# Optimization experiments

Hardware: AMD Instinct MI355X
Metric: run time of the kernel (lower is better)

Reference implementation:

```python
import jax, jax.numpy as jnp
import numpy as np

S, B, H = 4096, 32, 512

def setup_inputs() -> dict:
    key = jax.random.key(0)
    k1, k2, k3, k4, k5 = jax.random.split(key, 5)
    hidden = jax.random.normal(k1, (1, B, H), dtype=jnp.float32)
    encoder_outputs = jax.random.normal(k2, (S, B, H), dtype=jnp.float32)
    embedding = jax.random.normal(k3, (S, B, 3), dtype=jnp.float32)
    # learned params (xavier-ish scale)
    bigram_matrix = jax.random.normal(k4, (H, H), dtype=jnp.float32) * (1.0 / np.sqrt(H))
    affect_matrix = jax.random.normal(k5, (H, 3), dtype=jnp.float32) * 0.1
    return {"hidden": hidden, "encoder_outputs": encoder_outputs,
            "embedding": embedding, "bigram_matrix": bigram_matrix,
            "affect_matrix": affect_matrix}

def reference(hidden, encoder_outputs, embedding, bigram_matrix, affect_matrix):
    # hidden: [1,B,H] -> [B,H] (view(-1) over single layer)
    h = hidden[0]
    # bigram-modulated encoder states:
    #   i == 0: enc[0]
    #   i  > 0: (enc[i-1] @ W_bigram) * enc[i]
    modulated = jnp.einsum('sbh,hk->sbk', encoder_outputs[:-1], bigram_matrix) * encoder_outputs[1:]
    bigram_hidden = jnp.concatenate([encoder_outputs[:1], modulated], axis=0)  # [S,B,H]
    # dot-attention energy per (b, s)
    e_dot = jnp.einsum('sbh,bh->bs', bigram_hidden, h)  # [B,S]
    # affect term: (h @ affect_matrix) . embedding[s,b]
    e_aff = jnp.einsum('bk,sbk->bs', jnp.einsum('bh,hk->bk', h, affect_matrix), embedding)
    attn = jax.nn.softmax(e_dot + e_aff, axis=-1)  # softmax over seq dim
    return attn[:, None, :]  # [B,1,S]
```

## Files before the change

### kernel.cpp

```cpp
#include <hip/hip_runtime.h>
#include <cstdint>
#include <cstddef>

#define S_DIM 4096
#define B_DIM 32
#define H_DIM 512
#define M_DIM (S_DIM * B_DIM)

typedef unsigned short u16;
typedef unsigned int u32;
typedef float f32x4 __attribute__((ext_vector_type(4)));
typedef __bf16 bf16x8 __attribute__((ext_vector_type(8)));

__device__ __forceinline__ u16 f2bf(float v) {
    union { float f; u32 u; } a; a.f = v;
    u32 r = a.u + 0x7fffu + ((a.u >> 16) & 1u);
    return (u16)(r >> 16);
}
__device__ __forceinline__ float bf2f(u16 b) {
    union { float f; u32 u; } a; a.u = ((u32)b) << 16; return a.f;
}
__device__ __forceinline__ void split_bf(float v, u16& h, u16& l) {
    h = f2bf(v);
    l = f2bf(v - bf2f(h));
}

__device__ __forceinline__ void gl2lds16(const void* g, void* l) {
    __builtin_amdgcn_global_load_lds(
        (const __attribute__((address_space(1))) unsigned int*)g,
        (__attribute__((address_space(3))) unsigned int*)l,
        16, 0, 0);
}

__global__ void prep_w(const float* __restrict__ W,
                       u16* __restrict__ Wh, u16* __restrict__ Wl) {
    int i = blockIdx.x * 256 + threadIdx.x;
    float w = W[i];
    u16 h, l;
    split_bf(w, h, l);
    Wh[i] = h; Wl[i] = l;
}

__global__ void prep_v(const float* __restrict__ enc,
                       const float* __restrict__ hid,
                       u16* __restrict__ vh, u16* __restrict__ vl,
                       int m_base, int m_count) {
    const size_t nq = (size_t)m_count * (H_DIM / 4);
    const size_t stride = (size_t)gridDim.x * 256;
    for (size_t i = blockIdx.x * 256 + threadIdx.x; i < nq; i += stride) {
        const size_t elem  = i * 4;
        const size_t gelem = (size_t)m_base * H_DIM + elem;
        const int k = (int)(gelem & (H_DIM - 1));
        const int b = (int)((gelem >> 9) & 31);
        const float4 e = *(const float4*)(enc + gelem);
        const float4 h = *(const float4*)(hid + b * H_DIM + k);
        float v0 = e.x * h.x, v1 = e.y * h.y, v2 = e.z * h.z, v3 = e.w * h.w;
        u16 h0,h1,h2,h3,l0,l1,l2,l3;
        split_bf(v0, h0, l0); split_bf(v1, h1, l1);
        split_bf(v2, h2, l2); split_bf(v3, h3, l3);
        ushort4 hw, lw;
        hw.x = h0; hw.y = h1; hw.z = h2; hw.w = h3;
        lw.x = l0; lw.y = l1; lw.z = l2; lw.w = l3;
        *(ushort4*)(vh + elem) = hw;
        *(ushort4*)(vl + elem) = lw;
    }
}

__global__ __launch_bounds__(256, 2) void bigram_gemm(
    const float* __restrict__ enc,
    const u16* __restrict__ vh, const u16* __restrict__ vl,
    const u16* __restrict__ Wh, const u16* __restrict__ Wl,
    float* __restrict__ Lp, int m_base)
{
    __shared__ u16 sAh[128 * 32];
    __shared__ u16 sAl[128 * 32];
    __shared__ u16 sBh[128 * 32];
    __shared__ u16 sBl[128 * 32];
    __shared__ float rowsum[2][128];

    const int tid  = threadIdx.x;
    const int wave = tid >> 6;
    const int lane = tid & 63;
    const int wr   = wave >> 1;
    const int wc   = wave & 1;
    const int jt   = blockIdx.x & 3;
    const int mt   = blockIdx.x >> 2;
    const int m0   = m_base + mt * 128;
    const int j0   = jt * 128;
    const int g    = lane >> 4;
    const int cl   = lane & 15;

    const int srow = wave * 32 + (lane >> 2);
    const int scol = (lane & 3) * 8;
    const size_t aoff0 = (size_t)(mt * 128 + srow) * H_DIM + scol;
    const size_t aoff1 = aoff0 + (size_t)16 * H_DIM;
    const size_t boff0 = (size_t)(j0 + srow) * H_DIM + scol;
    const size_t boff1 = boff0 + (size_t)16 * H_DIM;
    const u16* pAh0 = vh + aoff0; const u16* pAh1 = vh + aoff1;
    const u16* pAl0 = vl + aoff0; const u16* pAl1 = vl + aoff1;
    const u16* pBh0 = Wh + boff0; const u16* pBh1 = Wh + boff1;
    const u16* pBl0 = Wl + boff0; const u16* pBl1 = Wl + boff1;
    const int d0 = wave * 1024, d1 = wave * 1024 + 512;

    f32x4 acc[4][4];
    #pragma unroll
    for (int mf = 0; mf < 4; ++mf)
        #pragma unroll
        for (int nf = 0; nf < 4; ++nf)
            acc[mf][nf] = (f32x4){0.f, 0.f, 0.f, 0.f};

    for (int kt = 0; kt < 16; ++kt) {
        const int ko = kt * 32;
        __syncthreads();
        gl2lds16(pAh0 + ko, sAh + d0);
        gl2lds16(pAh1 + ko, sAh + d1);
        gl2lds16(pAl0 + ko, sAl + d0);
        gl2lds16(pAl1 + ko, sAl + d1);
        gl2lds16(pBh0 + ko, sBh + d0);
        gl2lds16(pBh1 + ko, sBh + d1);
        gl2lds16(pBl0 + ko, sBl + d0);
        gl2lds16(pBl1 + ko, sBl + d1);
        __syncthreads();

        bf16x8 ah[4], al[4], bh[4], bl[4];
        #pragma unroll
        for (int mf = 0; mf < 4; ++mf) {
            const int ar = wr * 64 + mf * 16 + cl;
            ah[mf] = *(const bf16x8*)(sAh + ar * 32 + g * 8);
            al[mf] = *(const bf16x8*)(sAl + ar * 32 + g * 8);
        }
        #pragma unroll
        for (int nf = 0; nf < 4; ++nf) {
            const int br = wc * 64 + nf * 16 + cl;
            bh[nf] = *(const bf16x8*)(sBh + br * 32 + g * 8);
            bl[nf] = *(const bf16x8*)(sBl + br * 32 + g * 8);
        }
        #pragma unroll
        for (int mf = 0; mf < 4; ++mf)
            #pragma unroll
            for (int nf = 0; nf < 4; ++nf) {
                acc[mf][nf] = __builtin_amdgcn_mfma_f32_16x16x32_bf16(ah[mf], bh[nf], acc[mf][nf], 0, 0, 0);
                acc[mf][nf] = __builtin_amdgcn_mfma_f32_16x16x32_bf16(ah[mf], bl[nf], acc[mf][nf], 0, 0, 0);
                acc[mf][nf] = __builtin_amdgcn_mfma_f32_16x16x32_bf16(al[mf], bh[nf], acc[mf][nf], 0, 0, 0);
            }
    }

    #pragma unroll
    for (int mf = 0; mf < 4; ++mf) {
        float rs0 = 0.f, rs1 = 0.f, rs2 = 0.f, rs3 = 0.f;
        const int growb = m0 + wr * 64 + mf * 16 + g * 4;
        #pragma unroll
        for (int nf = 0; nf < 4; ++nf) {
            const int gcol = j0 + wc * 64 + nf * 16 + cl;
            float e0 = (growb + 0 >= B_DIM) ? enc[(size_t)(growb + 0 - B_DIM) * H_DIM + gcol] : 0.f;
            float e1 = (growb + 1 >= B_DIM) ? enc[(size_t)(growb + 1 - B_DIM) * H_DIM + gcol] : 0.f;
            float e2 = (growb + 2 >= B_DIM) ? enc[(size_t)(growb + 2 - B_DIM) * H_DIM + gcol] : 0.f;
            float e3 = (growb + 3 >= B_DIM) ? enc[(size_t)(growb + 3 - B_DIM) * H_DIM + gcol] : 0.f;
            rs0 += acc[mf][nf][0] * e0;
            rs1 += acc[mf][nf][1] * e1;
            rs2 += acc[mf][nf][2] * e2;
            rs3 += acc[mf][nf][3] * e3;
        }
        #pragma unroll
        for (int off = 1; off < 16; off <<= 1) {
            rs0 += __shfl_xor(rs0, off);
            rs1 += __shfl_xor(rs1, off);
            rs2 += __shfl_xor(rs2, off);
            rs3 += __shfl_xor(rs3, off);
        }
        if (cl == 0) {
            const int rb = wr * 64 + mf * 16 + g * 4;
            rowsum[wc][rb + 0] = rs0;
            rowsum[wc][rb + 1] = rs1;
            rowsum[wc][rb + 2] = rs2;
            rowsum[wc][rb + 3] = rs3;
        }
    }
    __syncthreads();
    if (tid < 128) {
        const int gm = m0 + tid;
        if (gm >= B_DIM) {
            Lp[(size_t)jt * M_DIM + (size_t)(gm & 31) * S_DIM + (gm >> 5)] =
                rowsum[0][tid] + rowsum[1][tid];
        }
    }
}

__global__ __launch_bounds__(256, 2) void bigram_gemm_direct(
    const float* __restrict__ enc,
    const float* __restrict__ hid,
    const u16* __restrict__ Wh,
    const u16* __restrict__ Wl,
    float* __restrict__ Lp)
{
    __shared__ float rowsum[2][128];
    const int tid  = threadIdx.x;
    const int wave = tid >> 6;
    const int lane = tid & 63;
    const int wr   = wave >> 1;
    const int wc   = wave & 1;
    const int jt   = blockIdx.x & 3;
    const int m0   = (blockIdx.x >> 2) * 128;
    const int j0   = jt * 128;
    const int g    = lane >> 4;
    const int cl   = lane & 15;

    f32x4 acc[4][4];
    #pragma unroll
    for (int mf = 0; mf < 4; ++mf)
        #pragma unroll
        for (int nf = 0; nf < 4; ++nf)
            acc[mf][nf] = (f32x4){0.f, 0.f, 0.f, 0.f};

    for (int kt = 0; kt < 8; ++kt) {
        #pragma unroll
        for (int kk = 0; kk < 2; ++kk) {
            const int k0 = kt * 64 + kk * 32 + g * 8;
            const float4 hA0 = *(const float4*)(hid + (size_t)cl * H_DIM + k0);
            const float4 hA1 = *(const float4*)(hid + (size_t)cl * H_DIM + k0 + 4);
            const float4 hB0 = *(const float4*)(hid + (size_t)(cl + 16) * H_DIM + k0);
            const float4 hB1 = *(const float4*)(hid + (size_t)(cl + 16) * H_DIM + k0 + 4);
            bf16x8 ah[4], al[4];
            #pragma unroll
            for (int mf = 0; mf < 4; ++mf) {
                const size_t rbase = (size_t)(m0 + wr * 64 + mf * 16 + cl) * H_DIM + k0;
                const float4 e0 = *(const float4*)(enc + rbase);
                const float4 e1 = *(const float4*)(enc + rbase + 4);
                const float4 h0 = (mf & 1) ? hB0 : hA0;
                const float4 h1 = (mf & 1) ? hB1 : hA1;
                float v[8];
                v[0] = e0.x * h0.x; v[1] = e0.y * h0.y; v[2] = e0.z * h0.z; v[3] = e0.w * h0.w;
                v[4] = e1.x * h1.x; v[5] = e1.y * h1.y; v[6] = e1.z * h1.z; v[7] = e1.w * h1.w;
                union { bf16x8 v8; u16 s[8]; } Hi, Lo;
                #pragma unroll
                for (int i = 0; i < 8; ++i) split_bf(v[i], Hi.s[i], Lo.s[i]);
                ah[mf] = Hi.v8;
                al[mf] = Lo.v8;
            }
            bf16x8 bh[4], bl[4];
            #pragma unroll
            for (int nf = 0; nf < 4; ++nf) {
                const size_t roff = (size_t)(j0 + wc * 64 + nf * 16 + cl) * H_DIM + k0;
                bh[nf] = *(const bf16x8*)(Wh + roff);
                bl[nf] = *(const bf16x8*)(Wl + roff);
            }
            #pragma unroll
            for (int mf = 0; mf < 4; ++mf)
                #pragma unroll
                for (int nf = 0; nf < 4; ++nf) {
                    acc[mf][nf] = __builtin_amdgcn_mfma_f32_16x16x32_bf16(ah[mf], bh[nf], acc[mf][nf], 0, 0, 0);
                    acc[mf][nf] = __builtin_amdgcn_mfma_f32_16x16x32_bf16(ah[mf], bl[nf], acc[mf][nf], 0, 0, 0);
                    acc[mf][nf] = __builtin_amdgcn_mfma_f32_16x16x32_bf16(al[mf], bh[nf], acc[mf][nf], 0, 0, 0);
                }
        }
    }

    #pragma unroll
    for (int mf = 0; mf < 4; ++mf) {
        float rs0 = 0.f, rs1 = 0.f, rs2 = 0.f, rs3 = 0.f;
        const int growb = m0 + wr * 64 + mf * 16 + g * 4;
        #pragma unroll
        for (int nf = 0; nf < 4; ++nf) {
            const int gcol = j0 + wc * 64 + nf * 16 + cl;
            float e0 = (growb + 0 >= B_DIM) ? enc[(size_t)(growb + 0 - B_DIM) * H_DIM + gcol] : 0.f;
            float e1 = (growb + 1 >= B_DIM) ? enc[(size_t)(growb + 1 - B_DIM) * H_DIM + gcol] : 0.f;
            float e2 = (growb + 2 >= B_DIM) ? enc[(size_t)(growb + 2 - B_DIM) * H_DIM + gcol] : 0.f;
            float e3 = (growb + 3 >= B_DIM) ? enc[(size_t)(growb + 3 - B_DIM) * H_DIM + gcol] : 0.f;
            rs0 += acc[mf][nf][0] * e0;
            rs1 += acc[mf][nf][1] * e1;
            rs2 += acc[mf][nf][2] * e2;
            rs3 += acc[mf][nf][3] * e3;
        }
        #pragma unroll
        for (int off = 1; off < 16; off <<= 1) {
            rs0 += __shfl_xor(rs0, off);
            rs1 += __shfl_xor(rs1, off);
            rs2 += __shfl_xor(rs2, off);
            rs3 += __shfl_xor(rs3, off);
        }
        if (cl == 0) {
            const int rb = wr * 64 + mf * 16 + g * 4;
            rowsum[wc][rb + 0] = rs0;
            rowsum[wc][rb + 1] = rs1;
            rowsum[wc][rb + 2] = rs2;
            rowsum[wc][rb + 3] = rs3;
        }
    }
    __syncthreads();
    if (tid < 128) {
        const int gm = m0 + tid;
        if (gm >= B_DIM) {
            Lp[(size_t)jt * M_DIM + (size_t)(gm & 31) * S_DIM + (gm >> 5)] =
                rowsum[0][tid] + rowsum[1][tid];
        }
    }
}

__global__ __launch_bounds__(1024) void softmax_kernel(
    const float* __restrict__ enc,
    const float* __restrict__ hid,
    const float* __restrict__ emb,
    const float* __restrict__ aff,
    const float* __restrict__ Lp,
    float* __restrict__ out)
{
    __shared__ float logits[S_DIM];
    __shared__ float wred[16][4];
    __shared__ float bcast[4];
    __shared__ float wtmp[16];

    const int b    = blockIdx.x;
    const int tid  = threadIdx.x;
    const int wave = tid >> 6;
    const int lane = tid & 63;

    float p0 = 0.f, p1 = 0.f, p2 = 0.f, p3 = 0.f;
    if (tid < H_DIM) {
        const int h = tid;
        const float hv = hid[b * H_DIM + h];
        p0 = hv * aff[h * 3 + 0];
        p1 = hv * aff[h * 3 + 1];
        p2 = hv * aff[h * 3 + 2];
        p3 = hv * enc[(size_t)b * H_DIM + h];
    }
    #pragma unroll
    for (int off = 32; off > 0; off >>= 1) {
        p0 += __shfl_down(p0, off);
        p1 += __shfl_down(p1, off);
        p2 += __shfl_down(p2, off);
        p3 += __shfl_down(p3, off);
    }
    if (lane == 0) { wred[wave][0] = p0; wred[wave][1] = p1; wred[wave][2] = p2; wred[wave][3] = p3; }
    __syncthreads();
    if (tid < 4) {
        float s = 0.f;
        #pragma unroll
        for (int w = 0; w < 16; ++w) s += wred[w][tid];
        bcast[tid] = s;
    }
    __syncthreads();
    const float ha0 = bcast[0], ha1 = bcast[1], ha2 = bcast[2], s0dot = bcast[3];

    float mx = -3.4e38f;
    #pragma unroll
    for (int it = 0; it < 4; ++it) {
        const int s = tid + it * 1024;
        const size_t base = (size_t)b * S_DIM + s;
        const float ed = (s == 0) ? s0dot
            : (Lp[base] + Lp[(size_t)M_DIM + base] + Lp[2 * (size_t)M_DIM + base] + Lp[3 * (size_t)M_DIM + base]);
        const float* e = emb + (size_t)(s * B_DIM + b) * 3;
        const float lg = ed + ha0 * e[0] + ha1 * e[1] + ha2 * e[2];
        logits[s] = lg;
        mx = fmaxf(mx, lg);
    }
    #pragma unroll
    for (int off = 32; off > 0; off >>= 1) mx = fmaxf(mx, __shfl_xor(mx, off));
    if (lane == 0) wtmp[wave] = mx;
    __syncthreads();
    mx = wtmp[0];
    #pragma unroll
    for (int w = 1; w < 16; ++w) mx = fmaxf(mx, wtmp[w]);
    __syncthreads();

    float sum = 0.f;
    #pragma unroll
    for (int it = 0; it < 4; ++it) {
        const int s = tid + it * 1024;
        const float ex = __expf(logits[s] - mx);
        logits[s] = ex;
        sum += ex;
    }
    #pragma unroll
    for (int off = 32; off > 0; off >>= 1) sum += __shfl_xor(sum, off);
    if (lane == 0) wtmp[wave] = sum;
    __syncthreads();
    sum = 0.f;
    #pragma unroll
    for (int w = 0; w < 16; ++w) sum += wtmp[w];
    const float inv = 1.0f / sum;
    #pragma unroll
    for (int it = 0; it < 4; ++it) {
        const int s = tid + it * 1024;
        out[(size_t)b * S_DIM + s] = logits[s] * inv;
    }
}

extern "C" void kernel_launch(void* const* d_in, const int* in_sizes, int n_in,
                              void* d_out, int out_size, void* d_ws, size_t ws_size,
                              hipStream_t stream) {
    const float* hid = (const float*)d_in[0];
    const float* enc = (const float*)d_in[1];
    const float* emb = (const float*)d_in[2];
    const float* Wm  = (const float*)d_in[3];
    const float* aff = (const float*)d_in[4];
    float* out = (float*)d_out;

    char* ws = (char*)d_ws;
    u16*   Wh = (u16*)ws;
    u16*   Wl = (u16*)(ws + (512u << 10));
    float* Lp = (float*)(ws + (1024u << 10));
    char*  vbase = ws + (1024u << 10) + (size_t)4 * M_DIM * 4;
    const size_t fixed = (1024u << 10) + (size_t)4 * M_DIM * 4;

    hipLaunchKernelGGL(prep_w, dim3(1024), dim3(256), 0, stream, Wm, Wh, Wl);

    const size_t avail = (ws_size > fixed) ? ws_size - fixed : 0;
    long chunk_m = (long)((avail / 2048) / 128) * 128;
    if (chunk_m > M_DIM) chunk_m = M_DIM;

    if (chunk_m >= 128) {
        u16* vh = (u16*)vbase;
        u16* vl = (u16*)(vbase + (size_t)chunk_m * H_DIM * sizeof(u16));
        for (long m_base = 0; m_base < M_DIM; m_base += chunk_m) {
            long mc = M_DIM - m_base;
            if (mc > chunk_m) mc = chunk_m;
            hipLaunchKernelGGL(prep_v, dim3((u32)(mc / 16)), dim3(256), 0, stream,
                               enc, hid, vh, vl, (int)m_base, (int)mc);
            hipLaunchKernelGGL(bigram_gemm, dim3((u32)((mc / 128) * 4)), dim3(256), 0, stream,
                               enc, vh, vl, Wh, Wl, Lp, (int)m_base);
        }
    } else {
        hipLaunchKernelGGL(bigram_gemm_direct, dim3(4096), dim3(256), 0, stream,
                           enc, hid, Wh, Wl, Lp);
    }

    hipLaunchKernelGGL(softmax_kernel, dim3(32), dim3(1024), 0, stream,
                       enc, hid, emb, aff, Lp, out);
}
```

Baseline: 646.0 us.

## Widen bigram GEMM tile to 128x256 using 32x32x16 MFMA

The bigram GEMM now gives each block a 128x256 output tile instead of 128x128, so only two column tiles cover H. The inner product uses 32x32x16 bf16 MFMA instructions in place of 16x16x32, and the epilogue reduction is adapted to the 32x32 accumulator layout. This halves redundant reloads of the A operand and the number of partial sums the softmax kernel must add, which now takes the partial count as a parameter. In exchange the kernel uses more LDS and registers per block, which can lower occupancy.

```diff
diff --git a/kernel.cpp b/kernel.cpp
--- a/kernel.cpp
+++ b/kernel.cpp
@@ -10,6 +10,7 @@
 typedef unsigned short u16;
 typedef unsigned int u32;
 typedef float f32x4 __attribute__((ext_vector_type(4)));
+typedef float f32x16 __attribute__((ext_vector_type(16)));
 typedef __bf16 bf16x8 __attribute__((ext_vector_type(8)));
 
 __device__ __forceinline__ u16 f2bf(float v) {
@@ -74,8 +75,8 @@
 {
     __shared__ u16 sAh[128 * 32];
     __shared__ u16 sAl[128 * 32];
-    __shared__ u16 sBh[128 * 32];
-    __shared__ u16 sBl[128 * 32];
+    __shared__ u16 sBh[256 * 32];
+    __shared__ u16 sBl[256 * 32];
     __shared__ float rowsum[2][128];
 
     const int tid  = threadIdx.x;
@@ -83,97 +84,96 @@
     const int lane = tid & 63;
     const int wr   = wave >> 1;
     const int wc   = wave & 1;
-    const int jt   = blockIdx.x & 3;
-    const int mt   = blockIdx.x >> 2;
+    const int jt   = blockIdx.x & 1;
+    const int mt   = blockIdx.x >> 1;
     const int m0   = m_base + mt * 128;
-    const int j0   = jt * 128;
-    const int g    = lane >> 4;
-    const int cl   = lane & 15;
-
-    const int srow = wave * 32 + (lane >> 2);
+    const int j0   = jt * 256;
+    const int l31  = lane & 31;
+    const int lh   = lane >> 5;
+
+    const int srow = lane >> 2;
     const int scol = (lane & 3) * 8;
-    const size_t aoff0 = (size_t)(mt * 128 + srow) * H_DIM + scol;
+    const size_t aoff0 = (size_t)(mt * 128 + wave * 32 + srow) * H_DIM + scol;
     const size_t aoff1 = aoff0 + (size_t)16 * H_DIM;
-    const size_t boff0 = (size_t)(j0 + srow) * H_DIM + scol;
-    const size_t boff1 = boff0 + (size_t)16 * H_DIM;
-    const u16* pAh0 = vh + aoff0; const u16* pAh1 = vh + aoff1;
-    const u16* pAl0 = vl + aoff0; const u16* pAl1 = vl + aoff1;
-    const u16* pBh0 = Wh + boff0; const u16* pBh1 = Wh + boff1;
-    const u16* pBl0 = Wl + boff0; const u16* pBl1 = Wl + boff1;
-    const int d0 = wave * 1024, d1 = wave * 1024 + 512;
-
-    f32x4 acc[4][4];
-    #pragma unroll
-    for (int mf = 0; mf < 4; ++mf)
-        #pragma unroll
-        for (int nf = 0; nf < 4; ++nf)
-            acc[mf][nf] = (f32x4){0.f, 0.f, 0.f, 0.f};
+    const size_t boff  = (size_t)(j0 + wave * 64 + srow) * H_DIM + scol;
+    const int da = wave * 1024;
+    const int db = wave * 2048;
+
+    f32x16 acc[2][4];
+    #pragma unroll
+    for (int rb = 0; rb < 2; ++rb)
+        #pragma unroll
+        for (int cb = 0; cb < 4; ++cb)
+            #pragma unroll
+            for (int r = 0; r < 16; ++r)
+                acc[rb][cb][r] = 0.f;
 
     for (int kt = 0; kt < 16; ++kt) {
         const int ko = kt * 32;
         __syncthreads();
-        gl2lds16(pAh0 + ko, sAh + d0);
-        gl2lds16(pAh1 + ko, sAh + d1);
-        gl2lds16(pAl0 + ko, sAl + d0);
-        gl2lds16(pAl1 + ko, sAl + d1);
-        gl2lds16(pBh0 + ko, sBh + d0);
-        gl2lds16(pBh1 + ko, sBh + d1);
-        gl2lds16(pBl0 + ko, sBl + d0);
-        gl2lds16(pBl1 + ko, sBl + d1);
+        gl2lds16(vh + aoff0 + ko, sAh + da);
+        gl2lds16(vh + aoff1 + ko, sAh + da + 512);
+        gl2lds16(vl + aoff0 + ko, sAl + da);
+        gl2lds16(vl + aoff1 + ko, sAl + da + 512);
+        #pragma unroll
+        for (int q = 0; q < 4; ++q) {
+            gl2lds16(Wh + boff + (size_t)(q * 16) * H_DIM + ko, sBh + db + q * 512);
+            gl2lds16(Wl + boff + (size_t)(q * 16) * H_DIM + ko, sBl + db + q * 512);
+        }
         __syncthreads();
 
-        bf16x8 ah[4], al[4], bh[4], bl[4];
-        #pragma unroll
-        for (int mf = 0; mf < 4; ++mf) {
-            const int ar = wr * 64 + mf * 16 + cl;
-            ah[mf] = *(const bf16x8*)(sAh + ar * 32 + g * 8);
-            al[mf] = *(const bf16x8*)(sAl + ar * 32 + g * 8);
-        }
-        #pragma unroll
-        for (int nf = 0; nf < 4; ++nf) {
-            const int br = wc * 64 + nf * 16 + cl;
-            bh[nf] = *(const bf16x8*)(sBh + br * 32 + g * 8);
-            bl[nf] = *(const bf16x8*)(sBl + br * 32 + g * 8);
-        }
-        #pragma unroll
-        for (int mf = 0; mf < 4; ++mf)
-            #pragma unroll
-            for (int nf = 0; nf < 4; ++nf) {
-                acc[mf][nf] = __builtin_amdgcn_mfma_f32_16x16x32_bf16(ah[mf], bh[nf], acc[mf][nf], 0, 0, 0);
-                acc[mf][nf] = __builtin_amdgcn_mfma_f32_16x16x32_bf16(ah[mf], bl[nf], acc[mf][nf], 0, 0, 0);
-                acc[mf][nf] = __builtin_amdgcn_mfma_f32_16x16x32_bf16(al[mf], bh[nf], acc[mf][nf], 0, 0, 0);
-            }
-    }
-
-    #pragma unroll
-    for (int mf = 0; mf < 4; ++mf) {
-        float rs0 = 0.f, rs1 = 0.f, rs2 = 0.f, rs3 = 0.f;
-        const int growb = m0 + wr * 64 + mf * 16 + g * 4;
-        #pragma unroll
-        for (int nf = 0; nf < 4; ++nf) {
-            const int gcol = j0 + wc * 64 + nf * 16 + cl;
-            float e0 = (growb + 0 >= B_DIM) ? enc[(size_t)(growb + 0 - B_DIM) * H_DIM + gcol] : 0.f;
-            float e1 = (growb + 1 >= B_DIM) ? enc[(size_t)(growb + 1 - B_DIM) * H_DIM + gcol] : 0.f;
-            float e2 = (growb + 2 >= B_DIM) ? enc[(size_t)(growb + 2 - B_DIM) * H_DIM + gcol] : 0.f;
-            float e3 = (growb + 3 >= B_DIM) ? enc[(size_t)(growb + 3 - B_DIM) * H_DIM + gcol] : 0.f;
-            rs0 += acc[mf][nf][0] * e0;
-            rs1 += acc[mf][nf][1] * e1;
-            rs2 += acc[mf][nf][2] * e2;
-            rs3 += acc[mf][nf][3] * e3;
-        }
-        #pragma unroll
-        for (int off = 1; off < 16; off <<= 1) {
-            rs0 += __shfl_xor(rs0, off);
-            rs1 += __shfl_xor(rs1, off);
-            rs2 += __shfl_xor(rs2, off);
-            rs3 += __shfl_xor(rs3, off);
-        }
-        if (cl == 0) {
-            const int rb = wr * 64 + mf * 16 + g * 4;
-            rowsum[wc][rb + 0] = rs0;
-            rowsum[wc][rb + 1] = rs1;
-            rowsum[wc][rb + 2] = rs2;
-            rowsum[wc][rb + 3] = rs3;
+        #pragma unroll
+        for (int ks = 0; ks < 2; ++ks) {
+            const int kb = ks * 16 + lh * 8;
+            bf16x8 ah[2], al[2], bh[4], bl[4];
+            #pragma unroll
+            for (int rb = 0; rb < 2; ++rb) {
+                const int row = wr * 64 + rb * 32 + l31;
+                ah[rb] = *(const bf16x8*)(sAh + row * 32 + kb);
+                al[rb] = *(const bf16x8*)(sAl + row * 32 + kb);
+            }
+            #pragma unroll
+            for (int cb = 0; cb < 4; ++cb) {
+                const int row = wc * 128 + cb * 32 + l31;
+                bh[cb] = *(const bf16x8*)(sBh + row * 32 + kb);
+                bl[cb] = *(const bf16x8*)(sBl + row * 32 + kb);
+            }
+            #pragma unroll
+            for (int rb = 0; rb < 2; ++rb)
+                #pragma unroll
+                for (int cb = 0; cb < 4; ++cb) {
+                    acc[rb][cb] = __builtin_amdgcn_mfma_f32_32x32x16_bf16(ah[rb], bh[cb], acc[rb][cb], 0, 0, 0);
+                    acc[rb][cb] = __builtin_amdgcn_mfma_f32_32x32x16_bf16(ah[rb], bl[cb], acc[rb][cb], 0, 0, 0);
+                    acc[rb][cb] = __builtin_amdgcn_mfma_f32_32x32x16_bf16(al[rb], bh[cb], acc[rb][cb], 0, 0, 0);
+                }
+        }
+    }
+
+    #pragma unroll
+    for (int rb = 0; rb < 2; ++rb) {
+        float t[16];
+        #pragma unroll
+        for (int r = 0; r < 16; ++r) {
+            const int rloc = (r & 3) + 8 * (r >> 2) + 4 * lh;
+            const int grow = m0 + wr * 64 + rb * 32 + rloc;
+            float tv = 0.f;
+            if (grow >= B_DIM) {
+                const float* ep = enc + (size_t)(grow - B_DIM) * H_DIM + j0 + wc * 128 + l31;
+                #pragma unroll
+                for (int cb = 0; cb < 4; ++cb)
+                    tv += acc[rb][cb][r] * ep[cb * 32];
+            }
+            #pragma unroll
+            for (int off = 1; off < 32; off <<= 1)
+                tv += __shfl_xor(tv, off);
+            t[r] = tv;
+        }
+        if (l31 == 0) {
+            #pragma unroll
+            for (int r = 0; r < 16; ++r) {
+                const int rloc = (r & 3) + 8 * (r >> 2) + 4 * lh;
+                rowsum[wc][wr * 64 + rb * 32 + rloc] = t[r];
+            }
         }
     }
     __syncthreads();
@@ -220,7 +220,8 @@
             const float4 hA1 = *(const float4*)(hid + (size_t)cl * H_DIM + k0 + 4);
             const float4 hB0 = *(const float4*)(hid + (size_t)(cl + 16) * H_DIM + k0);
             const float4 hB1 = *(const float4*)(hid + (size_t)(cl + 16) * H_DIM + k0 + 4);
-            bf16x8 ah[4], al[4];
+            typedef __bf16 bf16x8_t __attribute__((ext_vector_type(8)));
+            bf16x8_t ah[4], al[4];
             #pragma unroll
             for (int mf = 0; mf < 4; ++mf) {
                 const size_t rbase = (size_t)(m0 + wr * 64 + mf * 16 + cl) * H_DIM + k0;
@@ -231,18 +232,18 @@
                 float v[8];
                 v[0] = e0.x * h0.x; v[1] = e0.y * h0.y; v[2] = e0.z * h0.z; v[3] = e0.w * h0.w;
                 v[4] = e1.x * h1.x; v[5] = e1.y * h1.y; v[6] = e1.z * h1.z; v[7] = e1.w * h1.w;
-                union { bf16x8 v8; u16 s[8]; } Hi, Lo;
+                union { bf16x8_t v8; u16 s[8]; } Hi, Lo;
                 #pragma unroll
                 for (int i = 0; i < 8; ++i) split_bf(v[i], Hi.s[i], Lo.s[i]);
                 ah[mf] = Hi.v8;
                 al[mf] = Lo.v8;
             }
-            bf16x8 bh[4], bl[4];
+            bf16x8_t bh[4], bl[4];
             #pragma unroll
             for (int nf = 0; nf < 4; ++nf) {
                 const size_t roff = (size_t)(j0 + wc * 64 + nf * 16 + cl) * H_DIM + k0;
-                bh[nf] = *(const bf16x8*)(Wh + roff);
-                bl[nf] = *(const bf16x8*)(Wl + roff);
+                bh[nf] = *(const bf16x8_t*)(Wh + roff);
+                bl[nf] = *(const bf16x8_t*)(Wl + roff);
             }
             #pragma unroll
             for (int mf = 0; mf < 4; ++mf)
@@ -302,7 +303,7 @@
     const float* __restrict__ emb,
     const float* __restrict__ aff,
     const float* __restrict__ Lp,
-    float* __restrict__ out)
+    float* __restrict__ out, int np)
 {
     __shared__ float logits[S_DIM];
     __shared__ float wred[16][4];
@@ -346,8 +347,12 @@
     for (int it = 0; it < 4; ++it) {
         const int s = tid + it * 1024;
         const size_t base = (size_t)b * S_DIM + s;
-        const float ed = (s == 0) ? s0dot
-            : (Lp[base] + Lp[(size_t)M_DIM + base] + Lp[2 * (size_t)M_DIM + base] + Lp[3 * (size_t)M_DIM + base]);
+        float ed;
+        if (s == 0) ed = s0dot;
+        else {
+            ed = 0.f;
+            for (int p = 0; p < np; ++p) ed += Lp[(size_t)p * M_DIM + base];
+        }
         const float* e = emb + (size_t)(s * B_DIM + b) * 3;
         const float lg = ed + ha0 * e[0] + ha1 * e[1] + ha2 * e[2];
         logits[s] = lg;
@@ -408,7 +413,9 @@
     long chunk_m = (long)((avail / 2048) / 128) * 128;
     if (chunk_m > M_DIM) chunk_m = M_DIM;
 
+    int np;
     if (chunk_m >= 128) {
+        np = 2;
         u16* vh = (u16*)vbase;
         u16* vl = (u16*)(vbase + (size_t)chunk_m * H_DIM * sizeof(u16));
         for (long m_base = 0; m_base < M_DIM; m_base += chunk_m) {
@@ -416,14 +423,15 @@
             if (mc > chunk_m) mc = chunk_m;
             hipLaunchKernelGGL(prep_v, dim3((u32)(mc / 16)), dim3(256), 0, stream,
                                enc, hid, vh, vl, (int)m_base, (int)mc);
-            hipLaunchKernelGGL(bigram_gemm, dim3((u32)((mc / 128) * 4)), dim3(256), 0, stream,
+            hipLaunchKernelGGL(bigram_gemm, dim3((u32)((mc / 128) * 2)), dim3(256), 0, stream,
                                enc, vh, vl, Wh, Wl, Lp, (int)m_base);
         }
     } else {
+        np = 4;
         hipLaunchKernelGGL(bigram_gemm_direct, dim3(4096), dim3(256), 0, stream,
                            enc, hid, Wh, Wl, Lp);
     }
 
     hipLaunchKernelGGL(softmax_kernel, dim3(32), dim3(1024), 0, stream,
-                       enc, hid, emb, aff, Lp, out);
-}
+                       enc, hid, emb, aff, Lp, out, np);
+}
```

Measured after the change: 704.4 us. +9.0%, slower.
